# Optimization experiments

Hardware: AMD Instinct MI355X
Metric: run time of the kernel (lower is better)

Reference implementation:

```python
import jax, jax.numpy as jnp
import numpy as np
from jax import lax

# 32 binary morphology kernels, row-major bit strings (kernel01..kernel800)
K3S = ["111001111", "111101101", "111100111", "101101111",
       "011101111", "111101011", "111101110", "110101111"]
K4S = ["0011000110011111", "1100100010011111", "1111100100010011", "1111100110001100",
       "1001100110011111", "1111000100011111", "1111100110011001", "1111100010001111"]
K5S = ["0001100001000011000111111", "1100010000100001000111111",
       "1111110001100001000011000", "1111110001000010000100011",
       "1111110000100001000011111", "1111100001000010000111111",
       "1111110001100011000110001", "1000110001100011000111111"]
K6S = ["000011000001000001000001100001111111", "110000100000100000100000100001111111",
       "111111100001100000100000100000110000", "111111100001000001000001000001000011",
       "111111100000100000100000100000111111", "111111000001000001000001000001111111",
       "111111100001100001100001100001100001", "100001100001100001100001100001111111"]

def _mk(strs, k):
    a = np.array([[int(c) for c in s] for s in strs], dtype=np.float32)
    return jnp.asarray(a.reshape(len(strs), 1, k, k))

# 'thick' mode: enumerate(start=1) vs set(range(32)) drops the LAST kernel (index 31)
GROUPS = [_mk(K3S, 3), _mk(K4S, 4), _mk(K5S, 5), _mk(K6S, 6)[:7]]

DIA = jnp.ones((1, 1, 3, 3), jnp.float32)
ERO = jnp.asarray([[0, 1, 0], [1, 0, 1], [0, 1, 0]], jnp.float32).reshape(1, 1, 3, 3)

def _conv(x, k, pad):
    return lax.conv_general_dilated(x, k, (1, 1), ((pad, pad), (pad, pad)),
                                    dimension_numbers=("NCHW", "OIHW", "NCHW"))

def _sig2(x, beta=0.5, alpha=10.0):
    # 1 / (1 + exp(-alpha*(x - beta)))
    return jax.nn.sigmoid(alpha * (x - beta))

def _endpoints_group(padded, kers):
    # batch all same-size kernels as output channels of one conv
    k = kers.shape[-1]
    pad = k // 2
    nc = _conv(padded, kers, pad)
    nc = nc[:, :, :padded.shape[2], :padded.shape[3]]  # crop (even-size kernels overshoot)
    # soft_threshold(nc, 1.0) * mask
    le = jax.nn.sigmoid(jnp.clip(-10.0 * (nc - 1.0), -10.0, 10.0)) * padded
    return le[:, :, 1:-1, 1:-1].sum(axis=1, keepdims=True)

def _cp_map(t):
    p = jnp.pad(t, ((0, 0), (0, 0), (1, 1), (1, 1)), constant_values=1.0)
    epss = _endpoints_group(p, GROUPS[0])
    for K in GROUPS[1:]:
        epss = epss + _endpoints_group(p, K)
    return _sig2(epss)

def _dilate(x):
    return jnp.clip(_conv(x, DIA, 1), 0.0, 1.0)

def _erode(x):
    t = _conv(x, ERO, 1)
    return _sig2(t / (t.max() + 1e-8), beta=0.7, alpha=10.0)

def _get_cp(t):
    return _dilate(_cp_map(t))

def _topo_loss(pred, gt, num_erosions):
    ge, pe = [gt], [pred]
    for _ in range(num_erosions):
        ge.append(_erode(ge[-1]))
        pe.append(_erode(pe[-1]))
    loss = jnp.float32(0.0)
    for i in range(num_erosions + 1):
        loss = loss + ((_get_cp(pe[i]) - _get_cp(ge[i])) ** 2).sum()
        loss = loss + ((_get_cp(pe[i].max() - pe[i]) - _get_cp(ge[i].max() - ge[i])) ** 2).sum()
    return loss / pred.shape[0]


def setup_inputs() -> dict:
    key = jax.random.key(0)
    k1, k2 = jax.random.split(key)
    B, H, W = 8, 512, 512
    pred = jax.random.uniform(k1, (B, 1, H, W), dtype=jnp.float32)
    gt = jax.random.uniform(k2, (B, 1, H, W), dtype=jnp.float32)
    return {"pred": pred, "gt": gt, "num_erosions": 2}


def reference(pred, gt, num_erosions):
    return _topo_loss(pred, gt, num_erosions)
```

## Files before the change

### kernel.cpp

```cpp
#include <hip/hip_runtime.h>
#include <hip/hip_fp16.h>
#include <cstdint>

static constexpr int B = 8;
static constexpr int H = 512;
static constexpr int W = 512;
static constexpr int HW = H * W;
static constexpr int NPIX = B * HW;
static constexpr int NB1 = 1024;
static constexpr int NBD = 1024;

static constexpr int N_INT = 30 * 14;
static constexpr int N_EDGE = 64 + 120;
static constexpr int GRID_X = N_INT + N_EDGE;

static constexpr float CC = 14.4269504088896f;

__device__ __forceinline__ float rcpf(float x) { return __builtin_amdgcn_rcpf(x); }
__device__ __forceinline__ float exp2f_n(float x) { return __builtin_amdgcn_exp2f(x); }

typedef __attribute__((ext_vector_type(2))) float f2;

__device__ __forceinline__ f2 mk2(float a, float b) { f2 r; r.x = a; r.y = b; return r; }
__device__ __forceinline__ f2 exp2_2(f2 v) {
    f2 r; r.x = exp2f_n(v.x); r.y = exp2f_n(v.y); return r;
}
__device__ __forceinline__ f2 rcp_2(f2 v) {
    f2 r; r.x = rcpf(v.x); r.y = rcpf(v.y); return r;
}
#if defined(__has_builtin)
#if __has_builtin(__builtin_elementwise_fma)
#define FMA2(a, b, c) __builtin_elementwise_fma((a), (b), (c))
#endif
#endif
#ifndef FMA2
__device__ __forceinline__ f2 fma2_(f2 a, f2 b, f2 c) {
    f2 r; r.x = fmaf(a.x, b.x, c.x); r.y = fmaf(a.y, b.y, c.y); return r;
}
#define FMA2(a, b, c) fma2_((a), (b), (c))
#endif

__device__ __forceinline__ float sig_cp(float x) {
    return rcpf(1.0f + exp2f_n(fmaf(x, -CC, 0.5f * CC)));
}
__device__ __forceinline__ float sig_er(float r) {
    return rcpf(1.0f + exp2f_n(fmaf(r, -CC, 0.7f * CC)));
}
__device__ __forceinline__ void pair_term2(f2 nc, f2 negA, f2 s2m,
                                           f2& sd, f2& sc) {
    const f2 CC2 = CC;
    const f2 one2 = 1.0f;
    f2 w = exp2_2(FMA2(nc, CC2, negA));
    sd += rcp_2(FMA2(w, s2m, one2));
    sc += w * rcp_2(w + s2m);
}
__device__ __forceinline__ void end_term2(f2 nc, f2& sd) {
    const f2 CC2 = CC;
    const f2 nCC2 = -CC;
    const f2 one2 = 1.0f;
    sd += rcp_2(one2 + exp2_2(FMA2(nc, CC2, nCC2)));
}
__device__ __forceinline__ float wave_max(float m) {
#pragma unroll
    for (int o = 32; o > 0; o >>= 1) m = fmaxf(m, __shfl_down(m, o, 64));
    return m;
}
__device__ __forceinline__ float wave_sum(float s) {
#pragma unroll
    for (int o = 32; o > 0; o >>= 1) s += __shfl_down(s, o, 64);
    return s;
}

union H4 {
    uint64_t u;
    __half2 h2[2];
    __half h[4];
};

struct NC2 {
    f2 n3[8], n4[8], n5[8], n6[7];
    f2 v;
};

template <int STRIDE>
__device__ __forceinline__ NC2 sweep2(const f2* rp) {
    NC2 o;
    f2 r2s, r3s, r4s;
    f2 cen0, cen1, cen2, cen3, cen4, cen5, cen6, cen7, cen8;
    {
        f2 c0 = rp[0], c1 = rp[1], c2 = rp[2], c3 = rp[3], c4 = rp[4], c5 = rp[5];
        f2 c45 = c4 + c5, c01 = c0 + c1;
        f2 S6 = (c01 + (c2 + c3)) + c45;
        o.n6[0] = c45; o.n6[1] = c01; o.n6[2] = S6; o.n6[3] = S6;
        o.n6[4] = S6;  o.n6[5] = S6;  o.n6[6] = S6;
    }
    rp += STRIDE;
    {
        f2 c0 = rp[0], c1 = rp[1], c2 = rp[2], c3 = rp[3], c4 = rp[4], c5 = rp[5];
        f2 c45 = c4 + c5, c12 = c1 + c2, c34 = c3 + c4;
        f2 S4 = c12 + c34, S5 = S4 + c5;
        f2 c15 = c1 + c5, c05 = c0 + c5, c14 = c1 + c4;
        o.n6[0] += c5;  o.n6[1] += c0;  o.n6[2] += c05; o.n6[3] += c05;
        o.n6[4] += c0;  o.n6[5] += c5;  o.n6[6] += c05;
        o.n5[0] = c45; o.n5[1] = c12; o.n5[2] = S5; o.n5[3] = S5;
        o.n5[4] = S5;  o.n5[5] = S5;  o.n5[6] = S5; o.n5[7] = c15;
        o.n4[0] = c34; o.n4[1] = c12; o.n4[2] = S4; o.n4[3] = S4;
        o.n4[4] = c14; o.n4[5] = S4;  o.n4[6] = S4; o.n4[7] = S4;
    }
    rp += STRIDE;
    {
        f2 c0 = rp[0], c1 = rp[1], c2 = rp[2], c3 = rp[3], c4 = rp[4], c5 = rp[5];
        f2 c05 = c0 + c5, c15 = c1 + c5, c14 = c1 + c4;
        r2s = (c2 + c3) + c4;
        cen0 = c2; cen1 = c3; cen2 = c4;
        o.n6[0] += c5;  o.n6[1] += c0;  o.n6[2] += c0;  o.n6[3] += c5;
        o.n6[4] += c0;  o.n6[5] += c5;  o.n6[6] += c05;
        o.n5[0] += c5;  o.n5[1] += c1;  o.n5[2] += c15; o.n5[3] += c15;
        o.n5[4] += c1;  o.n5[5] += c5;  o.n5[6] += c15; o.n5[7] += c15;
        o.n4[0] += c4;  o.n4[1] += c1;  o.n4[2] += c14; o.n4[3] += c14;
        o.n4[4] += c14; o.n4[5] += c4;  o.n4[6] += c14; o.n4[7] += c1;
    }
    rp += STRIDE;
    {
        f2 c0 = rp[0], c1 = rp[1], c2 = rp[2], c3 = rp[3], c4 = rp[4], c5 = rp[5];
        f2 c05 = c0 + c5, c15 = c1 + c5, c14 = c1 + c4;
        r3s = (c2 + c3) + c4;
        cen3 = c2; cen4 = c3; cen5 = c4;
        o.v = c3;
        o.n6[0] += c5;  o.n6[1] += c0;  o.n6[2] += c0;  o.n6[3] += c5;
        o.n6[4] += c0;  o.n6[5] += c5;  o.n6[6] += c05;
        o.n5[0] += c5;  o.n5[1] += c1;  o.n5[2] += c1;  o.n5[3] += c5;
        o.n5[4] += c1;  o.n5[5] += c5;  o.n5[6] += c15; o.n5[7] += c15;
        o.n4[0] += c14; o.n4[1] += c14; o.n4[2] += c4;  o.n4[3] += c1;
        o.n4[4] += c14; o.n4[5] += c4;  o.n4[6] += c14; o.n4[7] += c1;
    }
    rp += STRIDE;
    {
        f2 c0 = rp[0], c1 = rp[1], c2 = rp[2], c3 = rp[3], c4 = rp[4], c5 = rp[5];
        f2 c05 = c0 + c5, c15 = c1 + c5, c12 = c1 + c2, c34 = c3 + c4;
        f2 S4 = c12 + c34, c14 = c1 + c4;
        r4s = (c2 + c3) + c4;
        cen6 = c2; cen7 = c3; cen8 = c4;
        o.n6[0] += c05; o.n6[1] += c05; o.n6[2] += c0;  o.n6[3] += c5;
        o.n6[4] += c0;  o.n6[5] += c5;  o.n6[6] += c05;
        o.n5[0] += c15; o.n5[1] += c15; o.n5[2] += c1;  o.n5[3] += c5;
        o.n5[4] += c1;  o.n5[5] += c5;  o.n5[6] += c15; o.n5[7] += c15;
        o.n4[0] += S4;  o.n4[1] += S4;  o.n4[2] += c34; o.n4[3] += c12;
        o.n4[4] += S4;  o.n4[5] += S4;  o.n4[6] += c14; o.n4[7] += S4;
    }
    rp += STRIDE;
    {
        f2 c0 = rp[0], c1 = rp[1], c2 = rp[2], c3 = rp[3], c4 = rp[4], c5 = rp[5];
        f2 c45 = c4 + c5, c12 = c1 + c2;
        f2 t = c3 + c45, S5 = c12 + t, S6 = S5 + c0;
        f2 c01 = c0 + c1, c05 = c0 + c5, c15 = c1 + c5;
        o.n6[0] += S6;  o.n6[1] += S6;  o.n6[2] += c01; o.n6[3] += c45;
        o.n6[4] += S6;  o.n6[5] += S6;  o.n6[6] += c05;
        o.n5[0] += S5;  o.n5[1] += S5;  o.n5[2] += c12; o.n5[3] += c45;
        o.n5[4] += S5;  o.n5[5] += S5;  o.n5[6] += c15; o.n5[7] += S5;
    }
    f2 S33 = (r2s + r3s) + r4s;
    f2 T = S33 - cen4;
    o.n3[0] = T - cen3; o.n3[1] = T - cen7; o.n3[2] = T - cen5; o.n3[3] = T - cen1;
    o.n3[4] = T - cen0; o.n3[5] = T - cen6; o.n3[6] = T - cen8; o.n3[7] = T - cen2;
    return o;
}

__constant__ __device__ const int CI4[8] = {1, 1, 1, 1, 2, 2, 2, 2};
__constant__ __device__ const int CI5[8] = {3, 3, 3, 3, 4, 4, 4, 4};
__constant__ __device__ const int CI6[7] = {4, 4, 4, 4, 5, 5, 5};

template <bool PAIR>
__device__ __forceinline__ void ssum_from_nc2(const NC2& a, const f2* negA,
                                              const f2* s2m, f2& sD, f2& sC) {
    f2 sd = 0.0f, sc = 0.0f;
#pragma unroll
    for (int k = 0; k < 8; k++) {
        if constexpr (PAIR) pair_term2(a.n3[k], negA[0], s2m[0], sd, sc);
        else end_term2(a.n3[k], sd);
    }
#pragma unroll
    for (int k = 0; k < 8; k++) {
        if constexpr (PAIR) pair_term2(a.n4[k], negA[CI4[k]], s2m[CI4[k]], sd, sc);
        else end_term2(a.n4[k], sd);
    }
#pragma unroll
    for (int k = 0; k < 8; k++) {
        if constexpr (PAIR) pair_term2(a.n5[k], negA[CI5[k]], s2m[CI5[k]], sd, sc);
        else end_term2(a.n5[k], sd);
    }
#pragma unroll
    for (int k = 0; k < 7; k++) {
        if constexpr (PAIR) pair_term2(a.n6[k], negA[CI6[k]], s2m[CI6[k]], sd, sc);
        else end_term2(a.n6[k], sd);
    }
    sD = sd;
    sC = sc;
}

__global__ void setup_consts_kernel(const float* __restrict__ S,
                                    float* __restrict__ CST) {
    int t = threadIdx.x;
    if (t < 36) {
        int lvl = t / 12, rem = t % 12, cls = rem >> 1, img = rem & 1;
        const float cntf[6] = {7.0f, 9.0f, 10.0f, 11.0f, 13.0f, 16.0f};
        float M = S[lvl + 3 * img];
        float cm = fmaf(cntf[cls] * M, CC, -CC);
        float m = 0.5f * (cm - CC);
        CST[lvl * 24 + cls * 2 + img] = -(CC + m);
        CST[lvl * 24 + 12 + cls * 2 + img] = exp2f_n(m);
    }
}

__global__ __launch_bounds__(256, 4) void cp_main_kernel(
    const float* __restrict__ x0P, const float* __restrict__ x0G,
    const float* __restrict__ x1P, const float* __restrict__ x1G,
    const float* __restrict__ x2P, const float* __restrict__ x2G,
    const float* __restrict__ S, const float* __restrict__ CST,
    int lvl_base, int plane_lvl0, __half* __restrict__ cp) {
    __shared__ f2 win[37][23];
    const int lvl = lvl_base + (blockIdx.z >> 3);
    const int b = blockIdx.z & 7;
    const float* xP = (lvl == 0) ? x0P : (lvl == 1) ? x1P : x2P;
    const float* xG = (lvl == 0) ? x0G : (lvl == 1) ? x1G : x2G;
    const float MP = S[lvl], MG = S[3 + lvl];
    __half* cpb = cp + (size_t)(4 * (lvl - plane_lvl0)) * NPIX;
    const int tid = threadIdx.y * 16 + threadIdx.x;
    const int ty = threadIdx.y, tx = threadIdx.x;
    const f2* cbase = (const f2*)(CST + lvl * 24);

    if (blockIdx.x < N_INT) {
        const int txB = 1 + (int)blockIdx.x % 30;
        const int tyB = 1 + (int)blockIdx.x / 30;
        const int ox0 = txB * 16, oy0 = tyB * 32;
        const float* pb = xP + b * HW + (oy0 - 3) * W + (ox0 - 3);
        const float* gb = xG + b * HW + (oy0 - 3) * W + (ox0 - 3);
        for (int i = tid; i < 37 * 21; i += 256) {
            int r = i / 21, c = i % 21;
            win[r][c] = mk2(pb[r * W + c], gb[r * W + c]);
        }
        __syncthreads();
        f2 negA[6], s2m[6];
#pragma unroll
        for (int c = 0; c < 6; c++) { negA[c] = cbase[c]; s2m[c] = cbase[6 + c]; }
        int o = b * HW + (oy0 + ty) * W + (ox0 + tx);
        {
            f2 sd, sc;
            NC2 a = sweep2<23>(&win[ty][tx]);
            ssum_from_nc2<true>(a, negA, s2m, sd, sc);
            H4 v;
            v.h[0] = __float2half(sig_cp(a.v.x * sd.x));
            v.h[1] = __float2half(sig_cp(a.v.y * sd.y));
            v.h[2] = __float2half(sig_cp((MP - a.v.x) * sc.x));
            v.h[3] = __float2half(sig_cp((MG - a.v.y) * sc.y));
            *(uint64_t*)(cpb + (size_t)o * 4) = v.u;
        }
        o += 16 * W;
        {
            f2 sd, sc;
            NC2 a = sweep2<23>(&win[ty + 16][tx]);
            ssum_from_nc2<true>(a, negA, s2m, sd, sc);
            H4 v;
            v.h[0] = __float2half(sig_cp(a.v.x * sd.x));
            v.h[1] = __float2half(sig_cp(a.v.y * sd.y));
            v.h[2] = __float2half(sig_cp((MP - a.v.x) * sc.x));
            v.h[3] = __float2half(sig_cp((MG - a.v.y) * sc.y));
            *(uint64_t*)(cpb + (size_t)o * 4) = v.u;
        }
    } else {
        const int e = (int)blockIdx.x - N_INT;
        int tx16, ty16;
        if (e < 64) {
            ty16 = e >> 1;
            tx16 = (e & 1) ? 31 : 0;
        } else {
            int e2 = e - 64;
            int r = e2 / 30;
            ty16 = (r == 0) ? 0 : (r == 1) ? 1 : (r == 2) ? 30 : 31;
            tx16 = 1 + e2 % 30;
        }
        const int ox0 = tx16 * 16, oy0 = ty16 * 16;
        const int o = b * HW + (oy0 + ty) * W + (ox0 + tx);
        const bool fastw = (tx16 >= 1) & (tx16 <= 30) & (ty16 >= 1) & (ty16 <= 30);
        if (fastw) {
            const float* pb = xP + b * HW + (oy0 - 3) * W + (ox0 - 3);
            const float* gb = xG + b * HW + (oy0 - 3) * W + (ox0 - 3);
            for (int i = tid; i < 21 * 21; i += 256) {
                int r = i / 21, c = i % 21;
                win[r][c] = mk2(pb[r * W + c], gb[r * W + c]);
            }
            __syncthreads();
            f2 negA[6], s2m[6], sd, sc;
#pragma unroll
            for (int c = 0; c < 6; c++) { negA[c] = cbase[c]; s2m[c] = cbase[6 + c]; }
            NC2 a = sweep2<23>(&win[ty][tx]);
            ssum_from_nc2<true>(a, negA, s2m, sd, sc);
            H4 v;
            v.h[0] = __float2half(sig_cp(a.v.x * sd.x));
            v.h[1] = __float2half(sig_cp(a.v.y * sd.y));
            v.h[2] = __float2half(sig_cp((MP - a.v.x) * sc.x));
            v.h[3] = __float2half(sig_cp((MG - a.v.y) * sc.y));
            *(uint64_t*)(cpb + (size_t)o * 4) = v.u;
        } else {
            const float* pb = xP + b * HW;
            const float* gb = xG + b * HW;
            for (int i = tid; i < 21 * 21; i += 256) {
                int r = i / 21, c = i % 21;
                int pr = oy0 - 2 + r;
                int pc = ox0 - 2 + c;
                f2 v;
                if (pr < 0 || pr > H + 1 || pc < 0 || pc > W + 1) {
                    v = 0.0f;
                } else if (pr == 0 || pr == H + 1 || pc == 0 || pc == W + 1) {
                    v = 1.0f;
                } else {
                    v = mk2(pb[(pr - 1) * W + (pc - 1)], gb[(pr - 1) * W + (pc - 1)]);
                }
                win[r][c] = v;
            }
            __syncthreads();
            f2 sd, sc, junk;
            NC2 a = sweep2<23>(&win[ty][tx]);
            ssum_from_nc2<false>(a, nullptr, nullptr, sd, junk);
            f2 vD = a.v;
            __half2* po = (__half2*)(cpb + (size_t)o * 4);
            po[0] = __halves2half2(__float2half(sig_cp(vD.x * sd.x)),
                                   __float2half(sig_cp(vD.y * sd.y)));
            __syncthreads();
            for (int i = tid; i < 21 * 21; i += 256) {
                int r = i / 21, c = i % 21;
                int pr = oy0 - 2 + r;
                int pc = ox0 - 2 + c;
                f2 v;
                if (pr < 0 || pr > H + 1 || pc < 0 || pc > W + 1) {
                    v = 0.0f;
                } else if (pr == 0 || pr == H + 1 || pc == 0 || pc == W + 1) {
                    v = 1.0f;
                } else {
                    v = mk2(MP - pb[(pr - 1) * W + (pc - 1)],
                            MG - gb[(pr - 1) * W + (pc - 1)]);
                }
                win[r][c] = v;
            }
            __syncthreads();
            NC2 ac = sweep2<23>(&win[ty][tx]);
            ssum_from_nc2<false>(ac, nullptr, nullptr, sc, junk);
            po[1] = __halves2half2(__float2half(sig_cp(ac.v.x * sc.x)),
                                   __float2half(sig_cp(ac.v.y * sc.y)));
        }
    }
}

__device__ __forceinline__ float4 h4_add(float4 a, uint64_t u) {
    H4 v; v.u = u;
    float2 p0 = __half22float2(v.h2[0]);
    float2 p1 = __half22float2(v.h2[1]);
    a.x += p0.x; a.y += p0.y; a.z += p1.x; a.w += p1.y;
    return a;
}

__global__ __launch_bounds__(256) void dil_diff2_kernel(
    const __half* __restrict__ cp, float* __restrict__ partial) {
    const int plane_grp = blockIdx.x >> 10;
    const int r = blockIdx.x & (NBD - 1);
    const __half* cpb = cp + (size_t)(4 * plane_grp) * NPIX;
    const int T = r * 256 + threadIdx.x;
    const int x = T & (W - 1);
    const int g = T >> 9;
    const int y0 = (g & 63) << 3;
    const int b = g >> 6;
    const __half* pb = cpb + (size_t)b * HW * 4;

    float4 rs[10];
#pragma unroll
    for (int j = 0; j < 10; j++) {
        int yy = y0 - 1 + j;
        float4 acc = make_float4(0.0f, 0.0f, 0.0f, 0.0f);
        if (yy >= 0 && yy < H) {
            const __half* row = pb + (size_t)yy * (W * 4);
            if (x > 0)
                acc = h4_add(acc, *(const uint64_t*)(row + (size_t)(x - 1) * 4));
            acc = h4_add(acc, *(const uint64_t*)(row + (size_t)x * 4));
            if (x < W - 1)
                acc = h4_add(acc, *(const uint64_t*)(row + (size_t)(x + 1) * 4));
        }
        rs[j] = acc;
    }

    float s = 0.0f;
#pragma unroll
    for (int i = 0; i < 8; i++) {
        float s0 = (rs[i].x + rs[i + 1].x) + rs[i + 2].x;
        float s1 = (rs[i].y + rs[i + 1].y) + rs[i + 2].y;
        float s2 = (rs[i].z + rs[i + 1].z) + rs[i + 2].z;
        float s3 = (rs[i].w + rs[i + 1].w) + rs[i + 2].w;
        float d1 = fminf(s0, 1.0f) - fminf(s1, 1.0f);
        float d2 = fminf(s2, 1.0f) - fminf(s3, 1.0f);
        s += fmaf(d1, d1, d2 * d2);
    }
    s = wave_sum(s);
    __shared__ float red[4];
    int tid = threadIdx.x;
    if ((tid & 63) == 0) red[tid >> 6] = s;
    __syncthreads();
    if (tid == 0) partial[blockIdx.x] = (red[0] + red[1]) + (red[2] + red[3]);
}

__device__ __forceinline__ void cross4(const float* __restrict__ xp, int idx,
                                       int y, int c, float4& ctr, float t[4]) {
    const float4* v = (const float4*)(xp + idx);
    ctr = v[0];
    float4 up = (y > 0) ? *(const float4*)(xp + idx - W)
                        : make_float4(0, 0, 0, 0);
    float4 dn = (y < H - 1) ? *(const float4*)(xp + idx + W)
                            : make_float4(0, 0, 0, 0);
    float lf = (c > 0) ? xp[idx - 1] : 0.0f;
    float rt = (c < W - 4) ? xp[idx + 4] : 0.0f;
    t[0] = (up.x + dn.x) + (lf + ctr.y);
    t[1] = (up.y + dn.y) + (ctr.x + ctr.z);
    t[2] = (up.z + dn.z) + (ctr.y + ctr.w);
    t[3] = (up.w + dn.w) + (ctr.z + rt);
}

__global__ __launch_bounds__(256) void cross_max_both_kernel(
    const float* __restrict__ xP, const float* __restrict__ xG,
    float4* __restrict__ partial) {
    float mtP = 0, mtG = 0, mrP = 0, mrG = 0;
    for (int T = blockIdx.x * 256 + threadIdx.x; T < NPIX / 4; T += NB1 * 256) {
        int idx = T * 4;
        int i = idx & (HW - 1);
        int y = i >> 9;
        int c = i & (W - 1);
        float4 ctr;
        float t[4];
        cross4(xP, idx, y, c, ctr, t);
        mtP = fmaxf(mtP, fmaxf(fmaxf(t[0], t[1]), fmaxf(t[2], t[3])));
        mrP = fmaxf(mrP, fmaxf(fmaxf(ctr.x, ctr.y), fmaxf(ctr.z, ctr.w)));
        cross4(xG, idx, y, c, ctr, t);
        mtG = fmaxf(mtG, fmaxf(fmaxf(t[0], t[1]), fmaxf(t[2], t[3])));
        mrG = fmaxf(mrG, fmaxf(fmaxf(ctr.x, ctr.y), fmaxf(ctr.z, ctr.w)));
    }
    mtP = wave_max(mtP); mtG = wave_max(mtG);
    mrP = wave_max(mrP); mrG = wave_max(mrG);
    __shared__ float red[4][4];
    int tid = threadIdx.x;
    if ((tid & 63) == 0) {
        int w = tid >> 6;
        red[w][0] = mtP; red[w][1] = mtG; red[w][2] = mrP; red[w][3] = mrG;
    }
    __syncthreads();
    if (tid == 0) {
        float4 r;
        r.x = fmaxf(fmaxf(red[0][0], red[1][0]), fmaxf(red[2][0], red[3][0]));
        r.y = fmaxf(fmaxf(red[0][1], red[1][1]), fmaxf(red[2][1], red[3][1]));
        r.z = fmaxf(fmaxf(red[0][2], red[1][2]), fmaxf(red[2][2], red[3][2]));
        r.w = fmaxf(fmaxf(red[0][3], red[1][3]), fmaxf(red[2][3], red[3][3]));
        partial[blockIdx.x] = r;
    }
}

__global__ __launch_bounds__(256) void erode_both_kernel(
    const float* __restrict__ xP, const float* __restrict__ xG,
    const float4* __restrict__ PM,
    float* __restrict__ yP, float* __restrict__ yG,
    float* ymaxP, float* ymaxG, float* rmaxP, float* rmaxG) {
    float a = 0, bm = 0, c4 = 0, d4 = 0;
    {
        int t = threadIdx.x;
#pragma unroll
        for (int k = 0; k < NB1 / 256; k++) {
            float4 p = PM[t + k * 256];
            a = fmaxf(a, p.x); bm = fmaxf(bm, p.y);
            c4 = fmaxf(c4, p.z); d4 = fmaxf(d4, p.w);
        }
        a = wave_max(a); bm = wave_max(bm); c4 = wave_max(c4); d4 = wave_max(d4);
        __shared__ float red[4][4];
        if ((t & 63) == 0) {
            int w = t >> 6;
            red[w][0] = a; red[w][1] = bm; red[w][2] = c4; red[w][3] = d4;
        }
        __syncthreads();
        a  = fmaxf(fmaxf(red[0][0], red[1][0]), fmaxf(red[2][0], red[3][0]));
        bm = fmaxf(fmaxf(red[0][1], red[1][1]), fmaxf(red[2][1], red[3][1]));
        c4 = fmaxf(fmaxf(red[0][2], red[1][2]), fmaxf(red[2][2], red[3][2]));
        d4 = fmaxf(fmaxf(red[0][3], red[1][3]), fmaxf(red[2][3], red[3][3]));
    }
    const float tP_max = a, tG_max = bm;
    const float invP = rcpf(tP_max + 1e-8f);
    const float invG = rcpf(tG_max + 1e-8f);

    const int T = blockIdx.x * 256 + threadIdx.x;
    if (T < NPIX / 4) {
        int idx = T * 4;
        int i = idx & (HW - 1);
        int y = i >> 9;
        int c = i & (W - 1);
        float4 ctr;
        float t[4], o[4];
        cross4(xP, idx, y, c, ctr, t);
#pragma unroll
        for (int k = 0; k < 4; k++) o[k] = sig_er(t[k] * invP);
        *(float4*)(yP + idx) = make_float4(o[0], o[1], o[2], o[3]);
        cross4(xG, idx, y, c, ctr, t);
#pragma unroll
        for (int k = 0; k < 4; k++) o[k] = sig_er(t[k] * invG);
        *(float4*)(yG + idx) = make_float4(o[0], o[1], o[2], o[3]);
    }
    if (blockIdx.x == 0 && threadIdx.x == 0) {
        *ymaxP = sig_er(tP_max * invP);
        *ymaxG = sig_er(tG_max * invG);
        *rmaxP = c4;
        *rmaxG = d4;
    }
}

__global__ __launch_bounds__(1024) void finalize_kernel(
    const float* __restrict__ PS, float* out) {
    int t = threadIdx.x;
    float s = PS[t] + PS[t + NBD] + PS[t + 2 * NBD];
    s = wave_sum(s);
    __shared__ float red[16];
    if ((t & 63) == 0) red[t >> 6] = s;
    __syncthreads();
    if (t == 0) {
        float tot = 0.0f;
#pragma unroll
        for (int i = 0; i < 16; i++) tot += red[i];
        out[0] = tot * (1.0f / (float)B);
    }
}

extern "C" void kernel_launch(void* const* d_in, const int* in_sizes, int n_in,
                              void* d_out, int out_size, void* d_ws, size_t ws_size,
                              hipStream_t stream) {
    (void)in_sizes; (void)n_in; (void)out_size;
    const float* pred = (const float*)d_in[0];
    const float* gt   = (const float*)d_in[1];
    float* out = (float*)d_out;

    float* S  = (float*)d_ws;
    float4* PM = (float4*)(S + 64);
    float* CST = S + 64;
    float* PS = S + 64 + 4 * NB1;
    float* P1 = PS + 3 * NBD;
    float* G1 = P1 + NPIX;
    float* P2 = G1 + NPIX;
    float* G2 = P2 + NPIX;
    __half* CP = (__half*)(G2 + NPIX);

    const size_t base_b = (size_t)(64 + 4 * NB1 + 3 * NBD) * 4 +
                          (size_t)4 * NPIX * 4;
    const bool merged = ws_size >= base_b + (size_t)12 * NPIX * 2;

    const dim3 b1(256), g1(NB1), gE(NPIX / 4 / 256);
    const dim3 b2(16, 16, 1);

    cross_max_both_kernel<<<g1, b1, 0, stream>>>(pred, gt, PM);
    erode_both_kernel<<<gE, b1, 0, stream>>>(pred, gt, PM, P1, G1,
                                             S + 1, S + 4, S + 0, S + 3);
    cross_max_both_kernel<<<g1, b1, 0, stream>>>(P1, G1, PM);
    erode_both_kernel<<<gE, b1, 0, stream>>>(P1, G1, PM, P2, G2,
                                             S + 2, S + 5, S + 12, S + 13);
    setup_consts_kernel<<<1, 64, 0, stream>>>(S, CST);

    if (merged) {
        cp_main_kernel<<<dim3(GRID_X, 1, 3 * B), b2, 0, stream>>>(
            pred, gt, P1, G1, P2, G2, S, CST, 0, 0, CP);
        dil_diff2_kernel<<<dim3(3 * NBD), b1, 0, stream>>>(CP, PS);
    } else {
        for (int lvl = 0; lvl < 3; lvl++) {
            cp_main_kernel<<<dim3(GRID_X, 1, B), b2, 0, stream>>>(
                pred, gt, P1, G1, P2, G2, S, CST, lvl, lvl, CP);
            dil_diff2_kernel<<<dim3(NBD), b1, 0, stream>>>(CP, PS + lvl * NBD);
        }
    }

    finalize_kernel<<<1, 1024, 0, stream>>>(PS, out);
}
```

Baseline: 267.0 us.

## Fuse erosion chain into cooperative kernel and widen dilation-diff per thread

Result: slower. 705.9 us (+164.4%).

```diff
diff --git a/kernel.cpp b/kernel.cpp
--- a/kernel.cpp
+++ b/kernel.cpp
@@ -1,6 +1,9 @@
 #include <hip/hip_runtime.h>
 #include <hip/hip_fp16.h>
+#include <hip/hip_cooperative_groups.h>
 #include <cstdint>
+
+namespace cg = cooperative_groups;
 
 static constexpr int B = 8;
 static constexpr int H = 512;
@@ -76,6 +79,16 @@
     __half2 h2[2];
     __half h[4];
 };
+
+__device__ __forceinline__ float4 h4_to_f4(uint64_t u) {
+    H4 v; v.u = u;
+    float2 p0 = __half22float2(v.h2[0]);
+    float2 p1 = __half22float2(v.h2[1]);
+    return make_float4(p0.x, p0.y, p1.x, p1.y);
+}
+__device__ __forceinline__ float4 f4_add(float4 a, float4 b) {
+    return make_float4(a.x + b.x, a.y + b.y, a.z + b.z, a.w + b.w);
+}
 
 struct NC2 {
     f2 n3[8], n4[8], n5[8], n6[7];
@@ -198,10 +211,132 @@
     sC = sc;
 }
 
-__global__ void setup_consts_kernel(const float* __restrict__ S,
-                                    float* __restrict__ CST) {
-    int t = threadIdx.x;
-    if (t < 36) {
+__device__ __forceinline__ void cross4(const float* __restrict__ xp, int idx,
+                                       int y, int c, float4& ctr, float t[4]) {
+    const float4* v = (const float4*)(xp + idx);
+    ctr = v[0];
+    float4 up = (y > 0) ? *(const float4*)(xp + idx - W)
+                        : make_float4(0, 0, 0, 0);
+    float4 dn = (y < H - 1) ? *(const float4*)(xp + idx + W)
+                            : make_float4(0, 0, 0, 0);
+    float lf = (c > 0) ? xp[idx - 1] : 0.0f;
+    float rt = (c < W - 4) ? xp[idx + 4] : 0.0f;
+    t[0] = (up.x + dn.x) + (lf + ctr.y);
+    t[1] = (up.y + dn.y) + (ctr.x + ctr.z);
+    t[2] = (up.z + dn.z) + (ctr.y + ctr.w);
+    t[3] = (up.w + dn.w) + (ctr.z + rt);
+}
+
+__device__ __forceinline__ void cmax_phase(const float* __restrict__ xP,
+                                           const float* __restrict__ xG,
+                                           float4* __restrict__ partial) {
+    float mtP = 0, mtG = 0, mrP = 0, mrG = 0;
+    for (int T = blockIdx.x * 256 + threadIdx.x; T < NPIX / 4; T += NB1 * 256) {
+        int idx = T * 4;
+        int i = idx & (HW - 1);
+        int y = i >> 9;
+        int c = i & (W - 1);
+        float4 ctr;
+        float t[4];
+        cross4(xP, idx, y, c, ctr, t);
+        mtP = fmaxf(mtP, fmaxf(fmaxf(t[0], t[1]), fmaxf(t[2], t[3])));
+        mrP = fmaxf(mrP, fmaxf(fmaxf(ctr.x, ctr.y), fmaxf(ctr.z, ctr.w)));
+        cross4(xG, idx, y, c, ctr, t);
+        mtG = fmaxf(mtG, fmaxf(fmaxf(t[0], t[1]), fmaxf(t[2], t[3])));
+        mrG = fmaxf(mrG, fmaxf(fmaxf(ctr.x, ctr.y), fmaxf(ctr.z, ctr.w)));
+    }
+    mtP = wave_max(mtP); mtG = wave_max(mtG);
+    mrP = wave_max(mrP); mrG = wave_max(mrG);
+    __shared__ float red[4][4];
+    int tid = threadIdx.x;
+    __syncthreads();
+    if ((tid & 63) == 0) {
+        int w = tid >> 6;
+        red[w][0] = mtP; red[w][1] = mtG; red[w][2] = mrP; red[w][3] = mrG;
+    }
+    __syncthreads();
+    if (tid == 0) {
+        float4 r;
+        r.x = fmaxf(fmaxf(red[0][0], red[1][0]), fmaxf(red[2][0], red[3][0]));
+        r.y = fmaxf(fmaxf(red[0][1], red[1][1]), fmaxf(red[2][1], red[3][1]));
+        r.z = fmaxf(fmaxf(red[0][2], red[1][2]), fmaxf(red[2][2], red[3][2]));
+        r.w = fmaxf(fmaxf(red[0][3], red[1][3]), fmaxf(red[2][3], red[3][3]));
+        partial[blockIdx.x] = r;
+    }
+}
+
+__device__ __forceinline__ void erode_phase(
+    const float* __restrict__ xP, const float* __restrict__ xG,
+    const float4* __restrict__ PM,
+    float* __restrict__ yP, float* __restrict__ yG,
+    float* ymaxP, float* ymaxG, float* rmaxP, float* rmaxG) {
+    float a = 0, bm = 0, c4 = 0, d4 = 0;
+    {
+        int t = threadIdx.x;
+#pragma unroll
+        for (int k = 0; k < NB1 / 256; k++) {
+            float4 p = PM[t + k * 256];
+            a = fmaxf(a, p.x); bm = fmaxf(bm, p.y);
+            c4 = fmaxf(c4, p.z); d4 = fmaxf(d4, p.w);
+        }
+        a = wave_max(a); bm = wave_max(bm); c4 = wave_max(c4); d4 = wave_max(d4);
+        __shared__ float red[4][4];
+        __syncthreads();
+        if ((t & 63) == 0) {
+            int w = t >> 6;
+            red[w][0] = a; red[w][1] = bm; red[w][2] = c4; red[w][3] = d4;
+        }
+        __syncthreads();
+        a  = fmaxf(fmaxf(red[0][0], red[1][0]), fmaxf(red[2][0], red[3][0]));
+        bm = fmaxf(fmaxf(red[0][1], red[1][1]), fmaxf(red[2][1], red[3][1]));
+        c4 = fmaxf(fmaxf(red[0][2], red[1][2]), fmaxf(red[2][2], red[3][2]));
+        d4 = fmaxf(fmaxf(red[0][3], red[1][3]), fmaxf(red[2][3], red[3][3]));
+    }
+    const float tP_max = a, tG_max = bm;
+    const float invP = rcpf(tP_max + 1e-8f);
+    const float invG = rcpf(tG_max + 1e-8f);
+
+    for (int T = blockIdx.x * 256 + threadIdx.x; T < NPIX / 4; T += NB1 * 256) {
+        int idx = T * 4;
+        int i = idx & (HW - 1);
+        int y = i >> 9;
+        int c = i & (W - 1);
+        float4 ctr;
+        float t[4], o[4];
+        cross4(xP, idx, y, c, ctr, t);
+#pragma unroll
+        for (int k = 0; k < 4; k++) o[k] = sig_er(t[k] * invP);
+        *(float4*)(yP + idx) = make_float4(o[0], o[1], o[2], o[3]);
+        cross4(xG, idx, y, c, ctr, t);
+#pragma unroll
+        for (int k = 0; k < 4; k++) o[k] = sig_er(t[k] * invG);
+        *(float4*)(yG + idx) = make_float4(o[0], o[1], o[2], o[3]);
+    }
+    if (blockIdx.x == 0 && threadIdx.x == 0) {
+        *ymaxP = sig_er(tP_max * invP);
+        *ymaxG = sig_er(tG_max * invG);
+        *rmaxP = c4;
+        *rmaxG = d4;
+    }
+}
+
+__global__ __launch_bounds__(256, 4) void erosion_chain_kernel(
+    const float* __restrict__ pred, const float* __restrict__ gt,
+    float* __restrict__ P1, float* __restrict__ G1,
+    float* __restrict__ P2, float* __restrict__ G2,
+    float4* PM, float* S) {
+    cg::grid_group grid = cg::this_grid();
+    cmax_phase(pred, gt, PM);
+    grid.sync();
+    erode_phase(pred, gt, PM, P1, G1, S + 1, S + 4, S + 0, S + 3);
+    grid.sync();
+    cmax_phase(P1, G1, PM);
+    grid.sync();
+    erode_phase(P1, G1, PM, P2, G2, S + 2, S + 5, S + 12, S + 13);
+    grid.sync();
+    if (blockIdx.x == 0 && threadIdx.x < 36) {
+        float* CST = (float*)PM;
+        int t = threadIdx.x;
         int lvl = t / 12, rem = t % 12, cls = rem >> 1, img = rem & 1;
         const float cntf[6] = {7.0f, 9.0f, 10.0f, 11.0f, 13.0f, 16.0f};
         float M = S[lvl + 3 * img];
@@ -235,9 +370,13 @@
         const int ox0 = txB * 16, oy0 = tyB * 32;
         const float* pb = xP + b * HW + (oy0 - 3) * W + (ox0 - 3);
         const float* gb = xG + b * HW + (oy0 - 3) * W + (ox0 - 3);
-        for (int i = tid; i < 37 * 21; i += 256) {
-            int r = i / 21, c = i % 21;
-            win[r][c] = mk2(pb[r * W + c], gb[r * W + c]);
+        {
+            int i = tid, r = tid / 21, c = tid - (tid / 21) * 21;
+            while (i < 37 * 21) {
+                win[r][c] = mk2(pb[r * W + c], gb[r * W + c]);
+                i += 256; c += 4; r += 12;
+                if (c >= 21) { c -= 21; r += 1; }
+            }
         }
         __syncthreads();
         f2 negA[6], s2m[6];
@@ -285,9 +424,13 @@
         if (fastw) {
             const float* pb = xP + b * HW + (oy0 - 3) * W + (ox0 - 3);
             const float* gb = xG + b * HW + (oy0 - 3) * W + (ox0 - 3);
-            for (int i = tid; i < 21 * 21; i += 256) {
-                int r = i / 21, c = i % 21;
-                win[r][c] = mk2(pb[r * W + c], gb[r * W + c]);
+            {
+                int i = tid, r = tid / 21, c = tid - (tid / 21) * 21;
+                while (i < 21 * 21) {
+                    win[r][c] = mk2(pb[r * W + c], gb[r * W + c]);
+                    i += 256; c += 4; r += 12;
+                    if (c >= 21) { c -= 21; r += 1; }
+                }
             }
             __syncthreads();
             f2 negA[6], s2m[6], sd, sc;
@@ -304,19 +447,23 @@
         } else {
             const float* pb = xP + b * HW;
             const float* gb = xG + b * HW;
-            for (int i = tid; i < 21 * 21; i += 256) {
-                int r = i / 21, c = i % 21;
-                int pr = oy0 - 2 + r;
-                int pc = ox0 - 2 + c;
-                f2 v;
-                if (pr < 0 || pr > H + 1 || pc < 0 || pc > W + 1) {
-                    v = 0.0f;
-                } else if (pr == 0 || pr == H + 1 || pc == 0 || pc == W + 1) {
-                    v = 1.0f;
-                } else {
-                    v = mk2(pb[(pr - 1) * W + (pc - 1)], gb[(pr - 1) * W + (pc - 1)]);
+            {
+                int i = tid, r = tid / 21, c = tid - (tid / 21) * 21;
+                while (i < 21 * 21) {
+                    int pr = oy0 - 2 + r;
+                    int pc = ox0 - 2 + c;
+                    f2 v;
+                    if (pr < 0 || pr > H + 1 || pc < 0 || pc > W + 1) {
+                        v = 0.0f;
+                    } else if (pr == 0 || pr == H + 1 || pc == 0 || pc == W + 1) {
+                        v = 1.0f;
+                    } else {
+                        v = mk2(pb[(pr - 1) * W + (pc - 1)], gb[(pr - 1) * W + (pc - 1)]);
+                    }
+                    win[r][c] = v;
+                    i += 256; c += 4; r += 12;
+                    if (c >= 21) { c -= 21; r += 1; }
                 }
-                win[r][c] = v;
             }
             __syncthreads();
             f2 sd, sc, junk;
@@ -327,20 +474,24 @@
             po[0] = __halves2half2(__float2half(sig_cp(vD.x * sd.x)),
                                    __float2half(sig_cp(vD.y * sd.y)));
             __syncthreads();
-            for (int i = tid; i < 21 * 21; i += 256) {
-                int r = i / 21, c = i % 21;
-                int pr = oy0 - 2 + r;
-                int pc = ox0 - 2 + c;
-                f2 v;
-                if (pr < 0 || pr > H + 1 || pc < 0 || pc > W + 1) {
-                    v = 0.0f;
-                } else if (pr == 0 || pr == H + 1 || pc == 0 || pc == W + 1) {
-                    v = 1.0f;
-                } else {
-                    v = mk2(MP - pb[(pr - 1) * W + (pc - 1)],
-                            MG - gb[(pr - 1) * W + (pc - 1)]);
+            {
+                int i = tid, r = tid / 21, c = tid - (tid / 21) * 21;
+                while (i < 21 * 21) {
+                    int pr = oy0 - 2 + r;
+                    int pc = ox0 - 2 + c;
+                    f2 v;
+                    if (pr < 0 || pr > H + 1 || pc < 0 || pc > W + 1) {
+                        v = 0.0f;
+                    } else if (pr == 0 || pr == H + 1 || pc == 0 || pc == W + 1) {
+                        v = 1.0f;
+                    } else {
+                        v = mk2(MP - pb[(pr - 1) * W + (pc - 1)],
+                                MG - gb[(pr - 1) * W + (pc - 1)]);
+                    }
+                    win[r][c] = v;
+                    i += 256; c += 4; r += 12;
+                    if (c >= 21) { c -= 21; r += 1; }
                 }
-                win[r][c] = v;
             }
             __syncthreads();
             NC2 ac = sweep2<23>(&win[ty][tx]);
@@ -351,52 +502,48 @@
     }
 }
 
-__device__ __forceinline__ float4 h4_add(float4 a, uint64_t u) {
-    H4 v; v.u = u;
-    float2 p0 = __half22float2(v.h2[0]);
-    float2 p1 = __half22float2(v.h2[1]);
-    a.x += p0.x; a.y += p0.y; a.z += p1.x; a.w += p1.y;
-    return a;
-}
-
-__global__ __launch_bounds__(256) void dil_diff2_kernel(
+__global__ __launch_bounds__(256, 4) void dil_diff2_kernel(
     const __half* __restrict__ cp, float* __restrict__ partial) {
-    const int plane_grp = blockIdx.x >> 10;
-    const int r = blockIdx.x & (NBD - 1);
+    const int plane_grp = blockIdx.x >> 9;
+    const int r = blockIdx.x & 511;
     const __half* cpb = cp + (size_t)(4 * plane_grp) * NPIX;
-    const int T = r * 256 + threadIdx.x;
-    const int x = T & (W - 1);
-    const int g = T >> 9;
-    const int y0 = (g & 63) << 3;
-    const int b = g >> 6;
+    const int x0 = threadIdx.x << 1;
+    const int y0 = (r & 63) << 3;
+    const int b = r >> 6;
     const __half* pb = cpb + (size_t)b * HW * 4;
 
-    float4 rs[10];
+    float4 ring0[3], ring1[3];
+    float s = 0.0f;
 #pragma unroll
     for (int j = 0; j < 10; j++) {
         int yy = y0 - 1 + j;
-        float4 acc = make_float4(0.0f, 0.0f, 0.0f, 0.0f);
+        float4 a0 = make_float4(0.f, 0.f, 0.f, 0.f);
+        float4 a1 = a0;
         if (yy >= 0 && yy < H) {
             const __half* row = pb + (size_t)yy * (W * 4);
-            if (x > 0)
-                acc = h4_add(acc, *(const uint64_t*)(row + (size_t)(x - 1) * 4));
-            acc = h4_add(acc, *(const uint64_t*)(row + (size_t)x * 4));
-            if (x < W - 1)
-                acc = h4_add(acc, *(const uint64_t*)(row + (size_t)(x + 1) * 4));
-        }
-        rs[j] = acc;
-    }
-
-    float s = 0.0f;
-#pragma unroll
-    for (int i = 0; i < 8; i++) {
-        float s0 = (rs[i].x + rs[i + 1].x) + rs[i + 2].x;
-        float s1 = (rs[i].y + rs[i + 1].y) + rs[i + 2].y;
-        float s2 = (rs[i].z + rs[i + 1].z) + rs[i + 2].z;
-        float s3 = (rs[i].w + rs[i + 1].w) + rs[i + 2].w;
-        float d1 = fminf(s0, 1.0f) - fminf(s1, 1.0f);
-        float d2 = fminf(s2, 1.0f) - fminf(s3, 1.0f);
-        s += fmaf(d1, d1, d2 * d2);
+            float4 f0 = h4_to_f4(*(const uint64_t*)(row + (size_t)x0 * 4));
+            float4 f1 = h4_to_f4(*(const uint64_t*)(row + (size_t)(x0 + 1) * 4));
+            float4 lf = make_float4(0.f, 0.f, 0.f, 0.f), rt = lf;
+            if (x0 > 0)
+                lf = h4_to_f4(*(const uint64_t*)(row + (size_t)(x0 - 1) * 4));
+            if (x0 + 2 < W)
+                rt = h4_to_f4(*(const uint64_t*)(row + (size_t)(x0 + 2) * 4));
+            a0 = f4_add(f4_add(lf, f0), f1);
+            a1 = f4_add(f4_add(f0, f1), rt);
+        }
+        ring0[j % 3] = a0; ring1[j % 3] = a1;
+        if (j >= 2) {
+            float4 v0 = f4_add(f4_add(ring0[(j - 2) % 3], ring0[(j - 1) % 3]),
+                               ring0[j % 3]);
+            float4 v1 = f4_add(f4_add(ring1[(j - 2) % 3], ring1[(j - 1) % 3]),
+                               ring1[j % 3]);
+            float d1 = fminf(v0.x, 1.0f) - fminf(v0.y, 1.0f);
+            float d2 = fminf(v0.z, 1.0f) - fminf(v0.w, 1.0f);
+            s += fmaf(d1, d1, d2 * d2);
+            d1 = fminf(v1.x, 1.0f) - fminf(v1.y, 1.0f);
+            d2 = fminf(v1.z, 1.0f) - fminf(v1.w, 1.0f);
+            s += fmaf(d1, d1, d2 * d2);
+        }
     }
     s = wave_sum(s);
     __shared__ float red[4];
@@ -406,118 +553,10 @@
     if (tid == 0) partial[blockIdx.x] = (red[0] + red[1]) + (red[2] + red[3]);
 }
 
-__device__ __forceinline__ void cross4(const float* __restrict__ xp, int idx,
-                                       int y, int c, float4& ctr, float t[4]) {
-    const float4* v = (const float4*)(xp + idx);
-    ctr = v[0];
-    float4 up = (y > 0) ? *(const float4*)(xp + idx - W)
-                        : make_float4(0, 0, 0, 0);
-    float4 dn = (y < H - 1) ? *(const float4*)(xp + idx + W)
-                            : make_float4(0, 0, 0, 0);
-    float lf = (c > 0) ? xp[idx - 1] : 0.0f;
-    float rt = (c < W - 4) ? xp[idx + 4] : 0.0f;
-    t[0] = (up.x + dn.x) + (lf + ctr.y);
-    t[1] = (up.y + dn.y) + (ctr.x + ctr.z);
-    t[2] = (up.z + dn.z) + (ctr.y + ctr.w);
-    t[3] = (up.w + dn.w) + (ctr.z + rt);
-}
-
-__global__ __launch_bounds__(256) void cross_max_both_kernel(
-    const float* __restrict__ xP, const float* __restrict__ xG,
-    float4* __restrict__ partial) {
-    float mtP = 0, mtG = 0, mrP = 0, mrG = 0;
-    for (int T = blockIdx.x * 256 + threadIdx.x; T < NPIX / 4; T += NB1 * 256) {
-        int idx = T * 4;
-        int i = idx & (HW - 1);
-        int y = i >> 9;
-        int c = i & (W - 1);
-        float4 ctr;
-        float t[4];
-        cross4(xP, idx, y, c, ctr, t);
-        mtP = fmaxf(mtP, fmaxf(fmaxf(t[0], t[1]), fmaxf(t[2], t[3])));
-        mrP = fmaxf(mrP, fmaxf(fmaxf(ctr.x, ctr.y), fmaxf(ctr.z, ctr.w)));
-        cross4(xG, idx, y, c, ctr, t);
-        mtG = fmaxf(mtG, fmaxf(fmaxf(t[0], t[1]), fmaxf(t[2], t[3])));
-        mrG = fmaxf(mrG, fmaxf(fmaxf(ctr.x, ctr.y), fmaxf(ctr.z, ctr.w)));
-    }
-    mtP = wave_max(mtP); mtG = wave_max(mtG);
-    mrP = wave_max(mrP); mrG = wave_max(mrG);
-    __shared__ float red[4][4];
-    int tid = threadIdx.x;
-    if ((tid & 63) == 0) {
-        int w = tid >> 6;
-        red[w][0] = mtP; red[w][1] = mtG; red[w][2] = mrP; red[w][3] = mrG;
-    }
-    __syncthreads();
-    if (tid == 0) {
-        float4 r;
-        r.x = fmaxf(fmaxf(red[0][0], red[1][0]), fmaxf(red[2][0], red[3][0]));
-        r.y = fmaxf(fmaxf(red[0][1], red[1][1]), fmaxf(red[2][1], red[3][1]));
-        r.z = fmaxf(fmaxf(red[0][2], red[1][2]), fmaxf(red[2][2], red[3][2]));
-        r.w = fmaxf(fmaxf(red[0][3], red[1][3]), fmaxf(red[2][3], red[3][3]));
-        partial[blockIdx.x] = r;
-    }
-}
-
-__global__ __launch_bounds__(256) void erode_both_kernel(
-    const float* __restrict__ xP, const float* __restrict__ xG,
-    const float4* __restrict__ PM,
-    float* __restrict__ yP, float* __restrict__ yG,
-    float* ymaxP, float* ymaxG, float* rmaxP, float* rmaxG) {
-    float a = 0, bm = 0, c4 = 0, d4 = 0;
-    {
-        int t = threadIdx.x;
-#pragma unroll
-        for (int k = 0; k < NB1 / 256; k++) {
-            float4 p = PM[t + k * 256];
-            a = fmaxf(a, p.x); bm = fmaxf(bm, p.y);
-            c4 = fmaxf(c4, p.z); d4 = fmaxf(d4, p.w);
-        }
-        a = wave_max(a); bm = wave_max(bm); c4 = wave_max(c4); d4 = wave_max(d4);
-        __shared__ float red[4][4];
-        if ((t & 63) == 0) {
-            int w = t >> 6;
-            red[w][0] = a; red[w][1] = bm; red[w][2] = c4; red[w][3] = d4;
-        }
-        __syncthreads();
-        a  = fmaxf(fmaxf(red[0][0], red[1][0]), fmaxf(red[2][0], red[3][0]));
-        bm = fmaxf(fmaxf(red[0][1], red[1][1]), fmaxf(red[2][1], red[3][1]));
-        c4 = fmaxf(fmaxf(red[0][2], red[1][2]), fmaxf(red[2][2], red[3][2]));
-        d4 = fmaxf(fmaxf(red[0][3], red[1][3]), fmaxf(red[2][3], red[3][3]));
-    }
-    const float tP_max = a, tG_max = bm;
-    const float invP = rcpf(tP_max + 1e-8f);
-    const float invG = rcpf(tG_max + 1e-8f);
-
-    const int T = blockIdx.x * 256 + threadIdx.x;
-    if (T < NPIX / 4) {
-        int idx = T * 4;
-        int i = idx & (HW - 1);
-        int y = i >> 9;
-        int c = i & (W - 1);
-        float4 ctr;
-        float t[4], o[4];
-        cross4(xP, idx, y, c, ctr, t);
-#pragma unroll
-        for (int k = 0; k < 4; k++) o[k] = sig_er(t[k] * invP);
-        *(float4*)(yP + idx) = make_float4(o[0], o[1], o[2], o[3]);
-        cross4(xG, idx, y, c, ctr, t);
-#pragma unroll
-        for (int k = 0; k < 4; k++) o[k] = sig_er(t[k] * invG);
-        *(float4*)(yG + idx) = make_float4(o[0], o[1], o[2], o[3]);
-    }
-    if (blockIdx.x == 0 && threadIdx.x == 0) {
-        *ymaxP = sig_er(tP_max * invP);
-        *ymaxG = sig_er(tG_max * invG);
-        *rmaxP = c4;
-        *rmaxG = d4;
-    }
-}
-
 __global__ __launch_bounds__(1024) void finalize_kernel(
     const float* __restrict__ PS, float* out) {
     int t = threadIdx.x;
-    float s = PS[t] + PS[t + NBD] + PS[t + 2 * NBD];
+    float s = PS[t] + ((t < 512) ? PS[t + 1024] : 0.0f);
     s = wave_sum(s);
     __shared__ float red[16];
     if ((t & 63) == 0) red[t >> 6] = s;
@@ -552,26 +591,25 @@
                           (size_t)4 * NPIX * 4;
     const bool merged = ws_size >= base_b + (size_t)12 * NPIX * 2;
 
-    const dim3 b1(256), g1(NB1), gE(NPIX / 4 / 256);
+    const dim3 b1(256);
     const dim3 b2(16, 16, 1);
 
-    cross_max_both_kernel<<<g1, b1, 0, stream>>>(pred, gt, PM);
-    erode_both_kernel<<<gE, b1, 0, stream>>>(pred, gt, PM, P1, G1,
-                                             S + 1, S + 4, S + 0, S + 3);
-    cross_max_both_kernel<<<g1, b1, 0, stream>>>(P1, G1, PM);
-    erode_both_kernel<<<gE, b1, 0, stream>>>(P1, G1, PM, P2, G2,
-                                             S + 2, S + 5, S + 12, S + 13);
-    setup_consts_kernel<<<1, 64, 0, stream>>>(S, CST);
+    {
+        void* kargs[] = {(void*)&pred, (void*)&gt, (void*)&P1, (void*)&G1,
+                         (void*)&P2, (void*)&G2, (void*)&PM, (void*)&S};
+        hipLaunchCooperativeKernel((const void*)erosion_chain_kernel,
+                                   dim3(NB1), b1, kargs, 0, stream);
+    }
 
     if (merged) {
         cp_main_kernel<<<dim3(GRID_X, 1, 3 * B), b2, 0, stream>>>(
             pred, gt, P1, G1, P2, G2, S, CST, 0, 0, CP);
-        dil_diff2_kernel<<<dim3(3 * NBD), b1, 0, stream>>>(CP, PS);
+        dil_diff2_kernel<<<dim3(3 * 512), b1, 0, stream>>>(CP, PS);
     } else {
         for (int lvl = 0; lvl < 3; lvl++) {
             cp_main_kernel<<<dim3(GRID_X, 1, B), b2, 0, stream>>>(
                 pred, gt, P1, G1, P2, G2, S, CST, lvl, lvl, CP);
-            dil_diff2_kernel<<<dim3(NBD), b1, 0, stream>>>(CP, PS + lvl * NBD);
+            dil_diff2_kernel<<<dim3(512), b1, 0, stream>>>(CP, PS + lvl * 512);
         }
     }
 
```
